# Performance work log

Hardware: AMD Instinct MI355X
Metric: run time of the kernel (lower is better)

## Reference

```python
import math
import jax, jax.numpy as jnp
import numpy as np

NUM_HEADS = 12
DIM = 1536
HEAD_DIM = DIM // NUM_HEADS  # 128
MAX_ATTN = 5632              # max_attention_size for window_size=(-1,-1)
EPS = 1e-6


def rmsnorm(x, g, eps=EPS):
    v = jnp.mean(jnp.square(x.astype(jnp.float32)), axis=-1, keepdims=True)
    return (x.astype(jnp.float32) * jax.lax.rsqrt(v + eps)).astype(x.dtype) * g


def causal_rope_apply(x, theta, start_frame, f, h, w):
    # x: [B, S, N, D] with S = f*h*w; theta: [1024, D//2] angles.
    b, s, n, d = x.shape
    c = d // 2
    ct = c - 2 * (c // 3)  # temporal rotary dims (22)
    ch = c // 3            # spatial rotary dims (21)
    ang = jnp.concatenate([
        jnp.broadcast_to(theta[start_frame:start_frame + f, :ct][:, None, None, :], (f, h, w, ct)),
        jnp.broadcast_to(theta[:h, ct:ct + ch][None, :, None, :], (f, h, w, ch)),
        jnp.broadcast_to(theta[:w, ct + ch:ct + 2 * ch][None, None, :, :], (f, h, w, ch)),
    ], axis=-1).reshape(s, c)
    cos = jnp.cos(ang)[None, :, None, :]  # [1, S, 1, c]
    sin = jnp.sin(ang)[None, :, None, :]
    xp = x.reshape(b, s, n, c, 2)
    xr, xi = xp[..., 0], xp[..., 1]
    out_r = xr * cos - xi * sin
    out_i = xr * sin + xi * cos
    return jnp.stack([out_r, out_i], axis=-1).reshape(b, s, n, d)


def setup_inputs() -> dict:
    key = jax.random.key(0)
    ks = jax.random.split(key, 12)
    B, F, H, W = 1, 2, 30, 52
    S = F * H * W  # 3120
    CACHE_LEN = 15600
    wscale = 0.02
    inp = {
        "x": jax.random.normal(ks[0], (B, S, DIM), jnp.float32),
        "freqs_theta": jax.random.uniform(ks[1], (1024, HEAD_DIM // 2), jnp.float32, 0.0, 2.0 * np.pi),
        "cache_k": jax.random.normal(ks[2], (B, CACHE_LEN, NUM_HEADS, HEAD_DIM), jnp.float32),
        "cache_v": jax.random.normal(ks[3], (B, CACHE_LEN, NUM_HEADS, HEAD_DIM), jnp.float32),
        "wq": jax.random.normal(ks[4], (DIM, DIM), jnp.float32) * wscale,
        "bq": jnp.zeros((DIM,), jnp.float32),
        "wk": jax.random.normal(ks[5], (DIM, DIM), jnp.float32) * wscale,
        "bk": jnp.zeros((DIM,), jnp.float32),
        "wv": jax.random.normal(ks[6], (DIM, DIM), jnp.float32) * wscale,
        "bv": jnp.zeros((DIM,), jnp.float32),
        "wo": jax.random.normal(ks[7], (DIM, DIM), jnp.float32) * wscale,
        "bo": jnp.zeros((DIM,), jnp.float32),
        "gq": jnp.ones((DIM,), jnp.float32),
        "gk": jnp.ones((DIM,), jnp.float32),
        "grid_f": F, "grid_h": H, "grid_w": W,
        "current_start": 7800,       # 5 frames already generated
        "global_end_index": 7800,
        "local_end_index": 7800,
    }
    return inp


def reference(x, freqs_theta, cache_k, cache_v, wq, bq, wk, bk, wv, bv, wo, bo,
              gq, gk, grid_f, grid_h, grid_w, current_start, global_end_index,
              local_end_index):
    B, S, D = x.shape
    N, Hd = NUM_HEADS, HEAD_DIM
    # qkv projections with RMS q/k norm (applied on full dim before head split)
    q = rmsnorm(x @ wq.T + bq, gq).reshape(B, S, N, Hd)
    k = rmsnorm(x @ wk.T + bk, gk).reshape(B, S, N, Hd)
    v = (x @ wv.T + bv).reshape(B, S, N, Hd)

    frame_seqlen = grid_h * grid_w
    start_frame = current_start // frame_seqlen
    rq = causal_rope_apply(q, freqs_theta, start_frame, grid_f, grid_h, grid_w)
    rk = causal_rope_apply(k, freqs_theta, start_frame, grid_f, grid_h, grid_w)

    # KV-cache scatter (static indices)
    current_end = current_start + S
    local_end = local_end_index + current_end - global_end_index
    local_start = local_end - S
    cache_k = cache_k.at[:, local_start:local_end].set(rk)
    cache_v = cache_v.at[:, local_start:local_end].set(v)

    # windowed attention over last MAX_ATTN cached tokens
    win_start = max(0, local_end - MAX_ATTN)
    kwin = cache_k[:, win_start:local_end]
    vwin = cache_v[:, win_start:local_end]
    scale = 1.0 / math.sqrt(Hd)
    scores = jnp.einsum('bqnd,bknd->bnqk', rq, kwin) * scale
    p = jax.nn.softmax(scores, axis=-1)
    o = jnp.einsum('bnqk,bknd->bqnd', p, vwin).reshape(B, S, D)
    return o @ wo.T + bo
```

## Files before the change

kernel.cpp:

```cpp
#include <hip/hip_runtime.h>

#define DIM 1536
#define NHEADS 12
#define HD 128
#define MAX_ATTN_WIN 5632
#define RMS_EPS 1e-6f
#define KWROWS 5632
#define NT_MAX 88
#define TILE_ELEMS 8192
#define KSTEPS 48
#define AREG 4096
#define BREG 8192

typedef unsigned short ushortT;
typedef __bf16 bf16x8 __attribute__((ext_vector_type(8)));
typedef float f32x4 __attribute__((ext_vector_type(4)));
typedef ushortT ushx8 __attribute__((ext_vector_type(8)));

__device__ __forceinline__ ushortT bf16r(float x) {
    union { float f; unsigned u; } v; v.f = x;
    unsigned r = v.u + 0x7FFFu + ((v.u >> 16) & 1u);
    return (ushortT)(r >> 16);
}
__device__ __forceinline__ ushx8 pack8(float4 a, float4 b) {
    ushx8 u;
    u[0] = bf16r(a.x); u[1] = bf16r(a.y); u[2] = bf16r(a.z); u[3] = bf16r(a.w);
    u[4] = bf16r(b.x); u[5] = bf16r(b.y); u[6] = bf16r(b.z); u[7] = bf16r(b.w);
    return u;
}

__device__ __forceinline__ void gload_lds16(const void* g, void* l) {
    typedef const __attribute__((address_space(1))) unsigned int GU;
    typedef __attribute__((address_space(3))) unsigned int LU;
    __builtin_amdgcn_global_load_lds((GU*)(unsigned long long)g,
                                     (LU*)(unsigned long long)l, 16, 0, 0);
}

__device__ __forceinline__ void pack_a_body(const float* __restrict__ X,
                                            ushortT* __restrict__ Ap,
                                            int M, int idx)
{
    int row = idx / 192, ch = idx - row * 192;
    int ks = ch >> 2, c = ch & 3;
    int mb = row >> 6, r = row & 63;
    ushx8 uh, ul;
    if (row < M) {
        const float* p = X + (size_t)row * DIM + (ch << 3);
        float4 a = *(const float4*)p;
        float4 b2 = *(const float4*)(p + 4);
        float xs[8] = {a.x, a.y, a.z, a.w, b2.x, b2.y, b2.z, b2.w};
        #pragma unroll
        for (int j = 0; j < 8; ++j) {
            ushortT hh = bf16r(xs[j]);
            union { unsigned u; float f; } w; w.u = ((unsigned)hh) << 16;
            uh[j] = hh; ul[j] = bf16r(xs[j] - w.f);
        }
    } else {
        #pragma unroll
        for (int j = 0; j < 8; ++j) { uh[j] = 0; ul[j] = 0; }
    }
    size_t base = (size_t)(mb * KSTEPS + ks) * AREG
                + r * 32 + ((c ^ ((r >> 1) & 3)) << 3);
    *(ushx8*)&Ap[base] = uh;
    *(ushx8*)&Ap[base + 2048] = ul;
}

__device__ __forceinline__ void pack_b_body(const float* __restrict__ W,
                                            ushortT* __restrict__ Bp, int idx)
{
    int row = idx / 192, ch = idx - row * 192;
    int ks = ch >> 2, c = ch & 3;
    int nb = row >> 7, rn = row & 127;
    const float* p = W + (size_t)row * DIM + (ch << 3);
    float4 a = *(const float4*)p;
    float4 b2 = *(const float4*)(p + 4);
    float xs[8] = {a.x, a.y, a.z, a.w, b2.x, b2.y, b2.z, b2.w};
    ushx8 uh, ul;
    #pragma unroll
    for (int j = 0; j < 8; ++j) {
        ushortT hh = bf16r(xs[j]);
        union { unsigned u; float f; } w; w.u = ((unsigned)hh) << 16;
        uh[j] = hh; ul[j] = bf16r(xs[j] - w.f);
    }
    size_t base = (size_t)(nb * KSTEPS + ks) * BREG
                + rn * 32 + ((c ^ ((rn >> 1) & 3)) << 3);
    *(ushx8*)&Bp[base] = uh;
    *(ushx8*)&Bp[base + 4096] = ul;
}

__global__ __launch_bounds__(256)
void pack1_kernel(const float* __restrict__ x, const float* __restrict__ wq,
                  const float* __restrict__ wk,
                  ushortT* __restrict__ Ap, ushortT* __restrict__ Bp0,
                  ushortT* __restrict__ Bp1, int M, int gA, int gB)
{
    int b = blockIdx.x;
    if (b < gA) {
        pack_a_body(x, Ap, M, b * 256 + threadIdx.x);
    } else if (b < gA + gB) {
        pack_b_body(wq, Bp0, (b - gA) * 256 + threadIdx.x);
    } else {
        pack_b_body(wk, Bp1, (b - gA - gB) * 256 + threadIdx.x);
    }
}

__global__ __launch_bounds__(256)
void pack2_kernel(const float* __restrict__ wv, const float* __restrict__ wo,
                  ushortT* __restrict__ Bp0, ushortT* __restrict__ Bp1, int gB)
{
    int b = blockIdx.x;
    if (b < gB) pack_b_body(wv, Bp0, b * 256 + threadIdx.x);
    else        pack_b_body(wo, Bp1, (b - gB) * 256 + threadIdx.x);
}

__global__ __launch_bounds__(256)
void pack_a_kernel(const float* __restrict__ X, ushortT* __restrict__ Ap,
                   int M, int Mpad)
{
    int idx = blockIdx.x * 256 + threadIdx.x;
    if (idx >= Mpad * 192) return;
    pack_a_body(X, Ap, M, idx);
}

template<int MODE>
__device__ __forceinline__
void gemm_body(const ushortT* __restrict__ Ap, const ushortT* __restrict__ Bp,
               const float* __restrict__ bias, float* __restrict__ C,
               ushortT* __restrict__ vwout, int M, int nmb, int orig,
               const int* __restrict__ p_cs, const int* __restrict__ p_ge,
               const int* __restrict__ p_le,
               ushortT (*As)[AREG], ushortT (*Bs)[BREG])
{
    const int tid = threadIdx.x;
    const int wid = tid >> 6, lane = tid & 63;
    const int lo = lane & 15, hi = lane >> 4;
    const int wm = wid >> 1, wn = wid & 1;

    const int nwg = nmb * (DIM / 128);
    const int xcd = orig & 7, linb = orig >> 3;
    const int qd = nwg >> 3, rr2 = nwg & 7;
    const int wg = (xcd < rr2 ? xcd * (qd + 1) : rr2 * (qd + 1) + (xcd - rr2) * qd) + linb;
    const int nb = wg / nmb, mb = wg - nb * nmb;
    const int m0 = mb << 6, n0 = nb << 7;

    f32x4 acc[2][4];
    #pragma unroll
    for (int i = 0; i < 2; ++i)
        #pragma unroll
        for (int j = 0; j < 4; ++j) acc[i][j] = (f32x4)(0.f);

    const ushortT* Asrc = Ap + (size_t)mb * (KSTEPS * AREG);
    const ushortT* Bsrc = Bp + (size_t)nb * (KSTEPS * BREG);
    const int lofs = lane << 3;
    const int aBase0 = (wid << 10) + lofs;
    const int aBase1 = aBase0 + 512;
    const int bBase  = (wid << 11) + lofs;

    gload_lds16(Asrc + aBase0, &As[0][aBase0]);
    gload_lds16(Asrc + aBase1, &As[0][aBase1]);
    #pragma unroll
    for (int i = 0; i < 4; ++i)
        gload_lds16(Bsrc + bBase + (i << 9), &Bs[0][bBase + (i << 9)]);

    const int cOff = ((hi ^ ((lo >> 1) & 3)) << 3);

    for (int ks = 0; ks < KSTEPS; ++ks) {
        const int b = ks & 1;
        __syncthreads();
        if (ks + 1 < KSTEPS) {
            const ushortT* as1 = Asrc + ((size_t)(ks + 1) << 12);
            const ushortT* bs1 = Bsrc + ((size_t)(ks + 1) << 13);
            gload_lds16(as1 + aBase0, &As[b ^ 1][aBase0]);
            gload_lds16(as1 + aBase1, &As[b ^ 1][aBase1]);
            #pragma unroll
            for (int i = 0; i < 4; ++i)
                gload_lds16(bs1 + bBase + (i << 9), &Bs[b ^ 1][bBase + (i << 9)]);
        }

        bf16x8 aH[2], aL[2];
        #pragma unroll
        for (int mf = 0; mf < 2; ++mf) {
            int r = (wm << 5) + (mf << 4) + lo;
            aH[mf] = *(const bf16x8*)&As[b][r * 32 + cOff];
            aL[mf] = *(const bf16x8*)&As[b][r * 32 + cOff + 2048];
        }
        #pragma unroll
        for (int nf = 0; nf < 4; ++nf) {
            int rn = (wn << 6) + (nf << 4) + lo;
            bf16x8 bH = *(const bf16x8*)&Bs[b][rn * 32 + cOff];
            bf16x8 bL = *(const bf16x8*)&Bs[b][rn * 32 + cOff + 4096];
            #pragma unroll
            for (int mf = 0; mf < 2; ++mf) {
                acc[mf][nf] = __builtin_amdgcn_mfma_f32_16x16x32_bf16(aH[mf], bH, acc[mf][nf], 0, 0, 0);
                acc[mf][nf] = __builtin_amdgcn_mfma_f32_16x16x32_bf16(aL[mf], bH, acc[mf][nf], 0, 0, 0);
                acc[mf][nf] = __builtin_amdgcn_mfma_f32_16x16x32_bf16(aH[mf], bL, acc[mf][nf], 0, 0, 0);
            }
        }
    }

    if (MODE == 0) {
        #pragma unroll
        for (int mf = 0; mf < 2; ++mf) {
            #pragma unroll
            for (int reg = 0; reg < 4; ++reg) {
                int gm = m0 + (wm << 5) + (mf << 4) + (hi << 2) + reg;
                if (gm < M) {
                    #pragma unroll
                    for (int nf = 0; nf < 4; ++nf) {
                        int gn = n0 + (wn << 6) + (nf << 4) + lo;
                        C[(size_t)gm * DIM + gn] = acc[mf][nf][reg] + bias[gn];
                    }
                }
            }
        }
    } else {
        const int S = M;
        const int local_end = p_le[0] + (p_cs[0] + S) - p_ge[0];
        int win_start = local_end - MAX_ATTN_WIN; if (win_start < 0) win_start = 0;
        const int vbase = (local_end - S) - win_start;
        #pragma unroll
        for (int mf = 0; mf < 2; ++mf) {
            #pragma unroll
            for (int reg = 0; reg < 4; ++reg) {
                int gm = m0 + (wm << 5) + (mf << 4) + (hi << 2) + reg;
                if (gm < M) {
                    #pragma unroll
                    for (int nf = 0; nf < 4; ++nf) {
                        int gn = n0 + (wn << 6) + (nf << 4) + lo;
                        int h2 = gn >> 7, d = gn & 127;
                        int pos = vbase + gm;
                        int tt = pos >> 6, w = pos & 63;
                        int swz = (((w >> 3) ^ (d & 7)) << 3) | (w & 7);
                        vwout[((size_t)h2 * NT_MAX + tt) * TILE_ELEMS + ((size_t)d << 6) + swz] =
                            bf16r(acc[mf][nf][reg] + bias[gn]);
                    }
                }
            }
        }
    }
}

__global__ __launch_bounds__(256, 3)
void gemm_qk_kernel(const ushortT* __restrict__ Ap,
                    const ushortT* __restrict__ BpQ, const ushortT* __restrict__ BpK,
                    const float* __restrict__ bq, const float* __restrict__ bk,
                    float* __restrict__ Cq, float* __restrict__ Ck,
                    int M, int nmb, int nwg)
{
    __shared__ __align__(16) ushortT As[2][AREG];
    __shared__ __align__(16) ushortT Bs[2][BREG];
    int gid = (int)blockIdx.x;
    if (gid < nwg)
        gemm_body<0>(Ap, BpQ, bq, Cq, nullptr, M, nmb, gid, nullptr, nullptr, nullptr, As, Bs);
    else
        gemm_body<0>(Ap, BpK, bk, Ck, nullptr, M, nmb, gid - nwg, nullptr, nullptr, nullptr, As, Bs);
}

template<int MODE>
__global__ __launch_bounds__(256, 3)
void gemm_single_kernel(const ushortT* __restrict__ Ap, const ushortT* __restrict__ Bp,
                        const float* __restrict__ bias, float* __restrict__ C,
                        ushortT* __restrict__ vwout, int M, int nmb,
                        const int* __restrict__ p_cs, const int* __restrict__ p_ge,
                        const int* __restrict__ p_le)
{
    __shared__ __align__(16) ushortT As[2][AREG];
    __shared__ __align__(16) ushortT Bs[2][BREG];
    gemm_body<MODE>(Ap, Bp, bias, C, vwout, M, nmb, (int)blockIdx.x,
                    p_cs, p_ge, p_le, As, Bs);
}

__global__ __launch_bounds__(256)
void rmsnorm_rope_kernel(float* __restrict__ qbuf, float* __restrict__ kbuf,
                         const float* __restrict__ gq, const float* __restrict__ gk,
                         const float* __restrict__ theta,
                         const int* __restrict__ p_gh, const int* __restrict__ p_gw,
                         const int* __restrict__ p_cs, int S)
{
    const int s = blockIdx.x;
    float* row = ((blockIdx.y == 0) ? qbuf : kbuf) + (size_t)s * DIM;
    const float* g = (blockIdx.y == 0) ? gq : gk;
    const int tid = threadIdx.x;

    float v[6];
    #pragma unroll
    for (int i = 0; i < 6; ++i) v[i] = row[tid * 6 + i];
    float ss = 0.f;
    #pragma unroll
    for (int i = 0; i < 6; ++i) ss += v[i] * v[i];
    #pragma unroll
    for (int off = 32; off > 0; off >>= 1) ss += __shfl_xor(ss, off, 64);

    __shared__ float red[4];
    if ((tid & 63) == 0) red[tid >> 6] = ss;
    __syncthreads();
    float tot = red[0] + red[1] + red[2] + red[3];
    float rs = rsqrtf(tot * (1.0f / DIM) + RMS_EPS);

    const int H = p_gh[0], W = p_gw[0];
    const int fs = p_cs[0] / (H * W);
    const int fr = s / (H * W);
    const int rem = s - fr * (H * W);
    const int hh = rem / W;
    const int ww = rem - hh * W;

    #pragma unroll
    for (int pi = 0; pi < 3; ++pi) {
        int p = tid * 3 + pi;
        int j = p & 63;
        float xr = v[pi * 2]     * rs * g[tid * 6 + pi * 2];
        float xi = v[pi * 2 + 1] * rs * g[tid * 6 + pi * 2 + 1];
        int rowi = (j < 22) ? (fs + fr) : ((j < 43) ? hh : ww);
        float ang = theta[rowi * 64 + j];
        float sn, cs;
        sincosf(ang, &sn, &cs);
        row[tid * 6 + pi * 2]     = xr * cs - xi * sn;
        row[tid * 6 + pi * 2 + 1] = xr * sn + xi * cs;
    }
}

__global__ __launch_bounds__(256)
void pack_kv_kernel(const float* __restrict__ cache_k, const float* __restrict__ k_lin,
                    const float* __restrict__ cache_v,
                    ushortT* __restrict__ kw, ushortT* __restrict__ vw,
                    const int* __restrict__ p_cs, const int* __restrict__ p_ge,
                    const int* __restrict__ p_le, int S)
{
    const int kt = blockIdx.x;
    const int local_end = p_le[0] + (p_cs[0] + S) - p_ge[0];
    int win_start = local_end - MAX_ATTN_WIN; if (win_start < 0) win_start = 0;
    const int L = local_end - win_start;
    const int cpart = (local_end - S) - win_start;

    if (blockIdx.y < NHEADS) {
        const int h = blockIdx.y;
        #pragma unroll
        for (int i = 0; i < 4; ++i) {
            int cid = (i << 8) + threadIdx.x;
            int r = cid >> 4, c = cid & 15;
            int pos = (kt << 6) + r;
            ushx8 u;
            if (pos < L) {
                const float* src = (pos < cpart)
                    ? &cache_k[(size_t)(win_start + pos) * DIM + h * HD + (c << 3)]
                    : &k_lin[(size_t)(pos - cpart) * DIM + h * HD + (c << 3)];
                float4 a = *(const float4*)src;
                float4 b = *(const float4*)(src + 4);
                u = pack8(a, b);
            } else {
                #pragma unroll
                for (int j = 0; j < 8; ++j) u[j] = 0;
            }
            *(ushx8*)&kw[(size_t)h * (KWROWS * HD) + (size_t)pos * HD + ((c ^ (r & 15)) << 3)] = u;
        }
    } else {
        const int h = blockIdx.y - NHEADS;
        const int tbase = kt << 6;
        if (tbase >= cpart && tbase + 64 <= L) return;

        __shared__ float tile[64 * 132];
        #pragma unroll
        for (int i = 0; i < 8; ++i) {
            int cid = (i << 8) + threadIdx.x;
            int r = cid >> 5, fc = cid & 31;
            int pos = tbase + r;
            float4 vv = (pos < cpart)
                ? *(const float4*)&cache_v[(size_t)(win_start + pos) * DIM + h * HD + (fc << 2)]
                : make_float4(0.f, 0.f, 0.f, 0.f);
            *(float4*)&tile[r * 132 + (fc << 2)] = vv;
        }
        __syncthreads();
        #pragma unroll
        for (int i = 0; i < 4; ++i) {
            int cid = (i << 8) + threadIdx.x;
            int d = cid >> 3, kc = cid & 7;
            int kglob = tbase + (kc << 3);
            ushx8 u;
            #pragma unroll
            for (int j = 0; j < 8; ++j)
                u[j] = bf16r(tile[((kc << 3) + j) * 132 + d]);
            size_t base = ((size_t)h * NT_MAX + kt) * TILE_ELEMS + ((size_t)d << 6)
                        + ((size_t)((kc ^ (d & 7)) << 3));
            if (kglob + 8 <= cpart) {
                *(ushx8*)&vw[base] = u;
            } else {
                #pragma unroll
                for (int j = 0; j < 8; ++j) {
                    int pos = kglob + j;
                    if (pos < cpart)      vw[base + j] = u[j];
                    else if (pos >= L)    vw[base + j] = 0;
                }
            }
        }
    }
}

__global__ __launch_bounds__(256, 3)
void attn_mfma5_kernel(const float* __restrict__ q_lin,
                       const ushortT* __restrict__ kw, const ushortT* __restrict__ vw,
                       float* __restrict__ obuf,
                       const int* __restrict__ p_cs, const int* __restrict__ p_ge,
                       const int* __restrict__ p_le, int S, int nqb)
{
    __shared__ __align__(16) ushortT Ks[TILE_ELEMS];
    __shared__ __align__(16) ushortT Vs[2][TILE_ELEMS];

    const int tid = threadIdx.x;
    const int wid = tid >> 6, lane = tid & 63;
    const int lo = lane & 15, hi = lane >> 4;

    const int nwg = nqb * NHEADS;
    const int orig = (int)blockIdx.x;
    const int xcd = orig & 7, linb = orig >> 3;
    const int qd = nwg >> 3, rr = nwg & 7;
    const int wg = (xcd < rr ? xcd * (qd + 1) : rr * (qd + 1) + (xcd - rr) * qd) + linb;
    const int h = wg / nqb;
    const int q0 = (wg - h * nqb) << 6;

    const int local_end = p_le[0] + (p_cs[0] + S) - p_ge[0];
    int win_start = local_end - MAX_ATTN_WIN; if (win_start < 0) win_start = 0;
    const int L = local_end - win_start;
    const int ntiles = (L + 63) >> 6;

    bf16x8 aQ[4];
    {
        int q = q0 + (wid << 4) + lo;
        if (q < S) {
            const float* qp = q_lin + (size_t)q * DIM + h * HD + (hi << 3);
            #pragma unroll
            for (int ks = 0; ks < 4; ++ks) {
                float4 a = *(const float4*)&qp[ks * 32];
                float4 b = *(const float4*)&qp[ks * 32 + 4];
                ushx8 u = pack8(a, b);
                aQ[ks] = *(bf16x8*)&u;
            }
        } else {
            ushx8 z;
            #pragma unroll
            for (int j = 0; j < 8; ++j) z[j] = 0;
            #pragma unroll
            for (int ks = 0; ks < 4; ++ks) aQ[ks] = *(bf16x8*)&z;
        }
    }

    f32x4 Oa[8];
    float lsum[4];
    #pragma unroll
    for (int i = 0; i < 8; ++i) Oa[i] = (f32x4)(0.f);
    #pragma unroll
    for (int i = 0; i < 4; ++i) lsum[i] = 0.f;

    const ushortT* kwp = kw + (size_t)h * (NT_MAX * TILE_ELEMS);
    const ushortT* vwp = vw + (size_t)h * (NT_MAX * TILE_ELEMS);
    const float scale = 0.08838834764831845f;
    const int pbase = wid << 11;
    const int sbase = (wid << 11) + (lane << 3);

    #pragma unroll
    for (int i = 0; i < 4; ++i) {
        gload_lds16(kwp + sbase + (i << 9), &Ks[sbase + (i << 9)]);
        gload_lds16(vwp + sbase + (i << 9), &Vs[0][sbase + (i << 9)]);
    }

    for (int t = 0; t < ntiles; ++t) {
        const int b = t & 1;
        __syncthreads();

        f32x4 Sa[4];
        #pragma unroll
        for (int nt = 0; nt < 4; ++nt) Sa[nt] = (f32x4)(0.f);
        #pragma unroll
        for (int nt = 0; nt < 4; ++nt) {
            const int kr = (nt << 4) + lo;
            #pragma unroll
            for (int ks = 0; ks < 4; ++ks) {
                bf16x8 bF = *(const bf16x8*)&Ks[kr * 128 + ((((ks << 2) + hi) ^ (kr & 15)) << 3)];
                Sa[nt] = __builtin_amdgcn_mfma_f32_16x16x32_bf16(aQ[ks], bF, Sa[nt], 0, 0, 0);
            }
        }

        __syncthreads();

        if (t + 1 < ntiles) {
            const ushortT* vsrc = vwp + ((size_t)(t + 1) << 13);
            ushortT* vdst = &Vs[b ^ 1][0];
            #pragma unroll
            for (int i = 0; i < 4; ++i)
                gload_lds16(vsrc + sbase + (i << 9), vdst + sbase + (i << 9));
        }

        const bool tail = (((t + 1) << 6) > L);
        #pragma unroll
        for (int nt = 0; nt < 4; ++nt) {
            #pragma unroll
            for (int reg = 0; reg < 4; ++reg) {
                float sv = Sa[nt][reg] * scale - 20.f;
                if (tail) {
                    int kg = (t << 6) + (nt << 4) + lo;
                    if (kg >= L) sv = -1e30f;
                }
                float p = __expf(sv);
                lsum[reg] += p;
                Sa[nt][reg] = p;
            }
        }

        #pragma unroll
        for (int nt = 0; nt < 4; ++nt) {
            #pragma unroll
            for (int reg = 0; reg < 4; ++reg) {
                int r = (hi << 2) + reg;
                int cc = (nt << 1) + (lo >> 3);
                Ks[pbase + (r << 6) + ((cc ^ (r & 7)) << 3) + (lo & 7)] = bf16r(Sa[nt][reg]);
            }
        }
        bf16x8 pF[2];
        #pragma unroll
        for (int ks = 0; ks < 2; ++ks)
            pF[ks] = *(const bf16x8*)&Ks[pbase + (lo << 6) + ((((ks << 2) + hi) ^ (lo & 7)) << 3)];

        asm volatile("s_waitcnt lgkmcnt(0)" ::: "memory");
        __builtin_amdgcn_sched_barrier(0);

        if (t + 1 < ntiles) {
            const ushortT* ksrc = kwp + ((size_t)(t + 1) << 13);
            #pragma unroll
            for (int i = 0; i < 4; ++i)
                gload_lds16(ksrc + sbase + (i << 9), &Ks[sbase + (i << 9)]);
        }

        #pragma unroll
        for (int nto = 0; nto < 8; ++nto) {
            const int d = (nto << 4) + lo;
            #pragma unroll
            for (int ks = 0; ks < 2; ++ks) {
                bf16x8 vF = *(const bf16x8*)&Vs[b][(d << 6) + ((((ks << 2) + hi) ^ (d & 7)) << 3)];
                Oa[nto] = __builtin_amdgcn_mfma_f32_16x16x32_bf16(pF[ks], vF, Oa[nto], 0, 0, 0);
            }
        }
    }

    #pragma unroll
    for (int reg = 0; reg < 4; ++reg) {
        #pragma unroll
        for (int off = 1; off < 16; off <<= 1)
            lsum[reg] += __shfl_xor(lsum[reg], off, 64);
    }
    #pragma unroll
    for (int reg = 0; reg < 4; ++reg) {
        int q = q0 + (wid << 4) + (hi << 2) + reg;
        if (q < S) {
            float inv = 1.f / lsum[reg];
            #pragma unroll
            for (int nto = 0; nto < 8; ++nto)
                obuf[(size_t)q * DIM + h * HD + (nto << 4) + lo] = Oa[nto][reg] * inv;
        }
    }
}

extern "C" void kernel_launch(void* const* d_in, const int* in_sizes, int n_in,
                              void* d_out, int out_size, void* d_ws, size_t ws_size,
                              hipStream_t stream)
{
    const float* x       = (const float*)d_in[0];
    const float* theta   = (const float*)d_in[1];
    const float* cache_k = (const float*)d_in[2];
    const float* cache_v = (const float*)d_in[3];
    const float* wq = (const float*)d_in[4];
    const float* bq = (const float*)d_in[5];
    const float* wk = (const float*)d_in[6];
    const float* bk = (const float*)d_in[7];
    const float* wv = (const float*)d_in[8];
    const float* bv = (const float*)d_in[9];
    const float* wo = (const float*)d_in[10];
    const float* bo = (const float*)d_in[11];
    const float* gq = (const float*)d_in[12];
    const float* gk = (const float*)d_in[13];
    const int* p_gh = (const int*)d_in[15];
    const int* p_gw = (const int*)d_in[16];
    const int* p_cs = (const int*)d_in[17];
    const int* p_ge = (const int*)d_in[18];
    const int* p_le = (const int*)d_in[19];

    const int S = in_sizes[0] / DIM;
    const int nmb = (S + 63) / 64;
    const int Mpad = nmb * 64;

    float* q_lin = (float*)d_ws;
    float* k_lin = q_lin + (size_t)S * DIM;
    float* o_buf = k_lin;
    ushortT* Ap  = (ushortT*)(k_lin + (size_t)S * DIM);
    ushortT* kw  = Ap;
    ushortT* vw  = Ap + (size_t)nmb * KSTEPS * AREG;
    ushortT* Bp0 = vw + (size_t)NHEADS * NT_MAX * TILE_ELEMS;
    ushortT* Bp1 = Bp0 + (size_t)NHEADS * KSTEPS * BREG;

    dim3 blk(256);
    const int nwgG = nmb * (DIM / 128);
    const int gA = (Mpad * 192) / 256;
    const int gB = (DIM * 192) / 256;

    pack1_kernel<<<gA + 2 * gB, blk, 0, stream>>>(x, wq, wk, Ap, Bp0, Bp1, S, gA, gB);
    gemm_qk_kernel<<<2 * nwgG, blk, 0, stream>>>(Ap, Bp0, Bp1, bq, bk,
                                                 q_lin, k_lin, S, nmb, nwgG);
    pack2_kernel<<<2 * gB, blk, 0, stream>>>(wv, wo, Bp0, Bp1, gB);
    gemm_single_kernel<1><<<nwgG, blk, 0, stream>>>(Ap, Bp0, bv, nullptr, vw,
                                                    S, nmb, p_cs, p_ge, p_le);

    rmsnorm_rope_kernel<<<dim3(S, 2), blk, 0, stream>>>(q_lin, k_lin, gq, gk, theta,
                                                        p_gh, p_gw, p_cs, S);

    pack_kv_kernel<<<dim3(NT_MAX, 2 * NHEADS), blk, 0, stream>>>(
        cache_k, k_lin, cache_v, kw, vw, p_cs, p_ge, p_le, S);

    const int nqb = (S + 63) / 64;
    attn_mfma5_kernel<<<dim3(nqb * NHEADS), blk, 0, stream>>>(
        q_lin, kw, vw, o_buf, p_cs, p_ge, p_le, S, nqb);

    pack_a_kernel<<<gA, blk, 0, stream>>>(o_buf, Ap, S, Mpad);
    gemm_single_kernel<0><<<nwgG, blk, 0, stream>>>(Ap, Bp1, bo, (float*)d_out, nullptr,
                                                    S, nmb, p_cs, p_ge, p_le);
}
```

Baseline: 681.2 us.

## Double query rows per attention workgroup to reuse K/V tiles

Each attention workgroup now handles 128 query rows instead of 64. Each wave owns two 16-row sub-blocks, so every K and V fragment read from LDS feeds two MFMAs. This halves global and LDS traffic for K/V per query and halves the number of workgroups. The cost is more registers per wave: occupancy drops to 2 blocks per SIMD, and there are fewer blocks (300) to spread across the CUs, so tail and balance effects are possible.

Result: slower. 712.6 us (+4.6%).

```diff
diff --git a/kernel.cpp b/kernel.cpp
--- a/kernel.cpp
+++ b/kernel.cpp
@@ -395,8 +395,8 @@
     }
 }
 
-__global__ __launch_bounds__(256, 3)
-void attn_mfma5_kernel(const float* __restrict__ q_lin,
+__global__ __launch_bounds__(256, 2)
+void attn_mfma6_kernel(const float* __restrict__ q_lin,
                        const ushortT* __restrict__ kw, const ushortT* __restrict__ vw,
                        float* __restrict__ obuf,
                        const int* __restrict__ p_cs, const int* __restrict__ p_ge,
@@ -415,16 +415,17 @@
     const int qd = nwg >> 3, rr = nwg & 7;
     const int wg = (xcd < rr ? xcd * (qd + 1) : rr * (qd + 1) + (xcd - rr) * qd) + linb;
     const int h = wg / nqb;
-    const int q0 = (wg - h * nqb) << 6;
+    const int q0 = (wg - h * nqb) << 7;
 
     const int local_end = p_le[0] + (p_cs[0] + S) - p_ge[0];
     int win_start = local_end - MAX_ATTN_WIN; if (win_start < 0) win_start = 0;
     const int L = local_end - win_start;
     const int ntiles = (L + 63) >> 6;
 
-    bf16x8 aQ[4];
-    {
-        int q = q0 + (wid << 4) + lo;
+    bf16x8 aQ[2][4];
+    #pragma unroll
+    for (int sub = 0; sub < 2; ++sub) {
+        int q = q0 + (wid << 5) + (sub << 4) + lo;
         if (q < S) {
             const float* qp = q_lin + (size_t)q * DIM + h * HD + (hi << 3);
             #pragma unroll
@@ -432,23 +433,26 @@
                 float4 a = *(const float4*)&qp[ks * 32];
                 float4 b = *(const float4*)&qp[ks * 32 + 4];
                 ushx8 u = pack8(a, b);
-                aQ[ks] = *(bf16x8*)&u;
+                aQ[sub][ks] = *(bf16x8*)&u;
             }
         } else {
             ushx8 z;
             #pragma unroll
             for (int j = 0; j < 8; ++j) z[j] = 0;
             #pragma unroll
-            for (int ks = 0; ks < 4; ++ks) aQ[ks] = *(bf16x8*)&z;
-        }
-    }
-
-    f32x4 Oa[8];
-    float lsum[4];
-    #pragma unroll
-    for (int i = 0; i < 8; ++i) Oa[i] = (f32x4)(0.f);
-    #pragma unroll
-    for (int i = 0; i < 4; ++i) lsum[i] = 0.f;
+            for (int ks = 0; ks < 4; ++ks) aQ[sub][ks] = *(bf16x8*)&z;
+        }
+    }
+
+    f32x4 Oa[2][8];
+    float lsum[2][4];
+    #pragma unroll
+    for (int sub = 0; sub < 2; ++sub) {
+        #pragma unroll
+        for (int i = 0; i < 8; ++i) Oa[sub][i] = (f32x4)(0.f);
+        #pragma unroll
+        for (int i = 0; i < 4; ++i) lsum[sub][i] = 0.f;
+    }
 
     const ushortT* kwp = kw + (size_t)h * (NT_MAX * TILE_ELEMS);
     const ushortT* vwp = vw + (size_t)h * (NT_MAX * TILE_ELEMS);
@@ -466,16 +470,17 @@
         const int b = t & 1;
         __syncthreads();
 
-        f32x4 Sa[4];
-        #pragma unroll
-        for (int nt = 0; nt < 4; ++nt) Sa[nt] = (f32x4)(0.f);
+        f32x4 Sa[2][4];
+        #pragma unroll
+        for (int nt = 0; nt < 4; ++nt) { Sa[0][nt] = (f32x4)(0.f); Sa[1][nt] = (f32x4)(0.f); }
         #pragma unroll
         for (int nt = 0; nt < 4; ++nt) {
             const int kr = (nt << 4) + lo;
             #pragma unroll
             for (int ks = 0; ks < 4; ++ks) {
                 bf16x8 bF = *(const bf16x8*)&Ks[kr * 128 + ((((ks << 2) + hi) ^ (kr & 15)) << 3)];
-                Sa[nt] = __builtin_amdgcn_mfma_f32_16x16x32_bf16(aQ[ks], bF, Sa[nt], 0, 0, 0);
+                Sa[0][nt] = __builtin_amdgcn_mfma_f32_16x16x32_bf16(aQ[0][ks], bF, Sa[0][nt], 0, 0, 0);
+                Sa[1][nt] = __builtin_amdgcn_mfma_f32_16x16x32_bf16(aQ[1][ks], bF, Sa[1][nt], 0, 0, 0);
             }
         }
 
@@ -491,33 +496,43 @@
 
         const bool tail = (((t + 1) << 6) > L);
         #pragma unroll
-        for (int nt = 0; nt < 4; ++nt) {
-            #pragma unroll
-            for (int reg = 0; reg < 4; ++reg) {
-                float sv = Sa[nt][reg] * scale - 20.f;
-                if (tail) {
-                    int kg = (t << 6) + (nt << 4) + lo;
-                    if (kg >= L) sv = -1e30f;
+        for (int sub = 0; sub < 2; ++sub) {
+            #pragma unroll
+            for (int nt = 0; nt < 4; ++nt) {
+                #pragma unroll
+                for (int reg = 0; reg < 4; ++reg) {
+                    float sv = Sa[sub][nt][reg] * scale - 20.f;
+                    if (tail) {
+                        int kg = (t << 6) + (nt << 4) + lo;
+                        if (kg >= L) sv = -1e30f;
+                    }
+                    float p = __expf(sv);
+                    lsum[sub][reg] += p;
+                    Sa[sub][nt][reg] = p;
                 }
-                float p = __expf(sv);
-                lsum[reg] += p;
-                Sa[nt][reg] = p;
-            }
-        }
-
-        #pragma unroll
-        for (int nt = 0; nt < 4; ++nt) {
-            #pragma unroll
-            for (int reg = 0; reg < 4; ++reg) {
-                int r = (hi << 2) + reg;
-                int cc = (nt << 1) + (lo >> 3);
-                Ks[pbase + (r << 6) + ((cc ^ (r & 7)) << 3) + (lo & 7)] = bf16r(Sa[nt][reg]);
-            }
-        }
-        bf16x8 pF[2];
-        #pragma unroll
-        for (int ks = 0; ks < 2; ++ks)
-            pF[ks] = *(const bf16x8*)&Ks[pbase + (lo << 6) + ((((ks << 2) + hi) ^ (lo & 7)) << 3)];
+            }
+        }
+
+        #pragma unroll
+        for (int sub = 0; sub < 2; ++sub) {
+            #pragma unroll
+            for (int nt = 0; nt < 4; ++nt) {
+                #pragma unroll
+                for (int reg = 0; reg < 4; ++reg) {
+                    int r = (hi << 2) + reg;
+                    int cc = (nt << 1) + (lo >> 3);
+                    Ks[pbase + (sub << 10) + (r << 6) + ((cc ^ (r & 7)) << 3) + (lo & 7)] =
+                        bf16r(Sa[sub][nt][reg]);
+                }
+            }
+        }
+        bf16x8 pF[2][2];
+        #pragma unroll
+        for (int sub = 0; sub < 2; ++sub)
+            #pragma unroll
+            for (int ks = 0; ks < 2; ++ks)
+                pF[sub][ks] = *(const bf16x8*)&Ks[pbase + (sub << 10) + (lo << 6)
+                                                 + ((((ks << 2) + hi) ^ (lo & 7)) << 3)];
 
         asm volatile("s_waitcnt lgkmcnt(0)" ::: "memory");
         __builtin_amdgcn_sched_barrier(0);
@@ -535,25 +550,29 @@
             #pragma unroll
             for (int ks = 0; ks < 2; ++ks) {
                 bf16x8 vF = *(const bf16x8*)&Vs[b][(d << 6) + ((((ks << 2) + hi) ^ (d & 7)) << 3)];
-                Oa[nto] = __builtin_amdgcn_mfma_f32_16x16x32_bf16(pF[ks], vF, Oa[nto], 0, 0, 0);
-            }
-        }
-    }
-
-    #pragma unroll
-    for (int reg = 0; reg < 4; ++reg) {
-        #pragma unroll
-        for (int off = 1; off < 16; off <<= 1)
-            lsum[reg] += __shfl_xor(lsum[reg], off, 64);
-    }
-    #pragma unroll
-    for (int reg = 0; reg < 4; ++reg) {
-        int q = q0 + (wid << 4) + (hi << 2) + reg;
-        if (q < S) {
-            float inv = 1.f / lsum[reg];
-            #pragma unroll
-            for (int nto = 0; nto < 8; ++nto)
-                obuf[(size_t)q * DIM + h * HD + (nto << 4) + lo] = Oa[nto][reg] * inv;
+                Oa[0][nto] = __builtin_amdgcn_mfma_f32_16x16x32_bf16(pF[0][ks], vF, Oa[0][nto], 0, 0, 0);
+                Oa[1][nto] = __builtin_amdgcn_mfma_f32_16x16x32_bf16(pF[1][ks], vF, Oa[1][nto], 0, 0, 0);
+            }
+        }
+    }
+
+    #pragma unroll
+    for (int sub = 0; sub < 2; ++sub) {
+        #pragma unroll
+        for (int reg = 0; reg < 4; ++reg) {
+            #pragma unroll
+            for (int off = 1; off < 16; off <<= 1)
+                lsum[sub][reg] += __shfl_xor(lsum[sub][reg], off, 64);
+        }
+        #pragma unroll
+        for (int reg = 0; reg < 4; ++reg) {
+            int q = q0 + (wid << 5) + (sub << 4) + (hi << 2) + reg;
+            if (q < S) {
+                float inv = 1.f / lsum[sub][reg];
+                #pragma unroll
+                for (int nto = 0; nto < 8; ++nto)
+                    obuf[(size_t)q * DIM + h * HD + (nto << 4) + lo] = Oa[sub][nto][reg] * inv;
+            }
         }
     }
 }
@@ -613,8 +632,8 @@
     pack_kv_kernel<<<dim3(NT_MAX, 2 * NHEADS), blk, 0, stream>>>(
         cache_k, k_lin, cache_v, kw, vw, p_cs, p_ge, p_le, S);
 
-    const int nqb = (S + 63) / 64;
-    attn_mfma5_kernel<<<dim3(nqb * NHEADS), blk, 0, stream>>>(
+    const int nqb = (S + 127) / 128;
+    attn_mfma6_kernel<<<dim3(nqb * NHEADS), blk, 0, stream>>>(
         q_lin, kw, vw, o_buf, p_cs, p_ge, p_le, S, nqb);
 
     pack_a_kernel<<<gA, blk, 0, stream>>>(o_buf, Ap, S, Mpad);
```

## Fuse QKV GEMMs, write K window from rmsnorm-rope, overlap wo packing with attention

Applied to the files above, without the earlier changes.

Packs wq/wk/wv in one launch and runs the Q, K and V projections as a single GEMM launch with three block ranges. The rmsnorm+RoPE kernel now converts the rotated K rows to bf16 and writes them straight into the swizzled attention K window, so the KV pack kernel only handles cached tokens and skips tiles made up entirely of new tokens. The wo weight packing is appended as extra blocks of the attention kernel to fill idle CUs. This removes launches and a full fp32 K round-trip, at the cost of extra shared memory in rmsnorm and a heavier, more mixed attention grid.

After: 656.7 us. 1.04x faster.

```diff
diff --git a/kernel.cpp b/kernel.cpp
--- a/kernel.cpp
+++ b/kernel.cpp
@@ -89,28 +89,18 @@
 }
 
 __global__ __launch_bounds__(256)
-void pack1_kernel(const float* __restrict__ x, const float* __restrict__ wq,
-                  const float* __restrict__ wk,
-                  ushortT* __restrict__ Ap, ushortT* __restrict__ Bp0,
-                  ushortT* __restrict__ Bp1, int M, int gA, int gB)
+void pack_all_kernel(const float* __restrict__ x, const float* __restrict__ wq,
+                     const float* __restrict__ wk, const float* __restrict__ wv,
+                     ushortT* __restrict__ Ap, ushortT* __restrict__ Bp0,
+                     ushortT* __restrict__ Bp1, ushortT* __restrict__ Bp2,
+                     int M, int gA, int gB)
 {
     int b = blockIdx.x;
-    if (b < gA) {
-        pack_a_body(x, Ap, M, b * 256 + threadIdx.x);
-    } else if (b < gA + gB) {
-        pack_b_body(wq, Bp0, (b - gA) * 256 + threadIdx.x);
-    } else {
-        pack_b_body(wk, Bp1, (b - gA - gB) * 256 + threadIdx.x);
-    }
-}
-
-__global__ __launch_bounds__(256)
-void pack2_kernel(const float* __restrict__ wv, const float* __restrict__ wo,
-                  ushortT* __restrict__ Bp0, ushortT* __restrict__ Bp1, int gB)
-{
-    int b = blockIdx.x;
-    if (b < gB) pack_b_body(wv, Bp0, b * 256 + threadIdx.x);
-    else        pack_b_body(wo, Bp1, (b - gB) * 256 + threadIdx.x);
+    if (b < gA) { pack_a_body(x, Ap, M, b * 256 + threadIdx.x); return; }
+    b -= gA;
+    if (b < gB)            pack_b_body(wq, Bp0, b * 256 + threadIdx.x);
+    else if (b < 2 * gB)   pack_b_body(wk, Bp1, (b - gB) * 256 + threadIdx.x);
+    else                   pack_b_body(wv, Bp2, (b - 2 * gB) * 256 + threadIdx.x);
 }
 
 __global__ __launch_bounds__(256)
@@ -241,19 +231,26 @@
 }
 
 __global__ __launch_bounds__(256, 3)
-void gemm_qk_kernel(const ushortT* __restrict__ Ap,
-                    const ushortT* __restrict__ BpQ, const ushortT* __restrict__ BpK,
-                    const float* __restrict__ bq, const float* __restrict__ bk,
-                    float* __restrict__ Cq, float* __restrict__ Ck,
-                    int M, int nmb, int nwg)
+void gemm_qkv_kernel(const ushortT* __restrict__ Ap,
+                     const ushortT* __restrict__ BpQ, const ushortT* __restrict__ BpK,
+                     const ushortT* __restrict__ BpV,
+                     const float* __restrict__ bq, const float* __restrict__ bk,
+                     const float* __restrict__ bv,
+                     float* __restrict__ Cq, float* __restrict__ Ck,
+                     ushortT* __restrict__ vw,
+                     int M, int nmb, int nwg,
+                     const int* __restrict__ p_cs, const int* __restrict__ p_ge,
+                     const int* __restrict__ p_le)
 {
     __shared__ __align__(16) ushortT As[2][AREG];
     __shared__ __align__(16) ushortT Bs[2][BREG];
     int gid = (int)blockIdx.x;
     if (gid < nwg)
         gemm_body<0>(Ap, BpQ, bq, Cq, nullptr, M, nmb, gid, nullptr, nullptr, nullptr, As, Bs);
+    else if (gid < 2 * nwg)
+        gemm_body<0>(Ap, BpK, bk, Ck, nullptr, M, nmb, gid - nwg, nullptr, nullptr, nullptr, As, Bs);
     else
-        gemm_body<0>(Ap, BpK, bk, Ck, nullptr, M, nmb, gid - nwg, nullptr, nullptr, nullptr, As, Bs);
+        gemm_body<1>(Ap, BpV, bv, nullptr, vw, M, nmb, gid - 2 * nwg, p_cs, p_ge, p_le, As, Bs);
 }
 
 template<int MODE>
@@ -272,14 +269,17 @@
 
 __global__ __launch_bounds__(256)
 void rmsnorm_rope_kernel(float* __restrict__ qbuf, float* __restrict__ kbuf,
+                         ushortT* __restrict__ kw,
                          const float* __restrict__ gq, const float* __restrict__ gk,
                          const float* __restrict__ theta,
                          const int* __restrict__ p_gh, const int* __restrict__ p_gw,
-                         const int* __restrict__ p_cs, int S)
+                         const int* __restrict__ p_cs, const int* __restrict__ p_ge,
+                         const int* __restrict__ p_le, int S)
 {
     const int s = blockIdx.x;
-    float* row = ((blockIdx.y == 0) ? qbuf : kbuf) + (size_t)s * DIM;
-    const float* g = (blockIdx.y == 0) ? gq : gk;
+    const bool isQ = (blockIdx.y == 0);
+    float* row = (isQ ? qbuf : kbuf) + (size_t)s * DIM;
+    const float* g = isQ ? gq : gk;
     const int tid = threadIdx.x;
 
     float v[6];
@@ -292,6 +292,7 @@
     for (int off = 32; off > 0; off >>= 1) ss += __shfl_xor(ss, off, 64);
 
     __shared__ float red[4];
+    __shared__ ushortT krow[DIM];
     if ((tid & 63) == 0) red[tid >> 6] = ss;
     __syncthreads();
     float tot = red[0] + red[1] + red[2] + red[3];
@@ -304,6 +305,7 @@
     const int hh = rem / W;
     const int ww = rem - hh * W;
 
+    float out[6];
     #pragma unroll
     for (int pi = 0; pi < 3; ++pi) {
         int p = tid * 3 + pi;
@@ -314,17 +316,35 @@
         float ang = theta[rowi * 64 + j];
         float sn, cs;
         sincosf(ang, &sn, &cs);
-        row[tid * 6 + pi * 2]     = xr * cs - xi * sn;
-        row[tid * 6 + pi * 2 + 1] = xr * sn + xi * cs;
+        out[pi * 2]     = xr * cs - xi * sn;
+        out[pi * 2 + 1] = xr * sn + xi * cs;
+    }
+
+    if (isQ) {
+        #pragma unroll
+        for (int i = 0; i < 6; ++i) row[tid * 6 + i] = out[i];
+    } else {
+        #pragma unroll
+        for (int i = 0; i < 6; ++i) krow[tid * 6 + i] = bf16r(out[i]);
+        __syncthreads();
+        const int local_end = p_le[0] + (p_cs[0] + S) - p_ge[0];
+        int win_start = local_end - MAX_ATTN_WIN; if (win_start < 0) win_start = 0;
+        const int cpart = (local_end - S) - win_start;
+        const int pos = cpart + s;
+        if (pos >= 0 && tid < 192) {
+            int h2 = tid >> 4, c = tid & 15;
+            ushx8 u = *(const ushx8*)&krow[h2 * 128 + (c << 3)];
+            *(ushx8*)&kw[(size_t)h2 * (KWROWS * HD) + (size_t)pos * HD
+                         + ((c ^ (pos & 15)) << 3)] = u;
+        }
     }
 }
 
 __global__ __launch_bounds__(256)
-void pack_kv_kernel(const float* __restrict__ cache_k, const float* __restrict__ k_lin,
-                    const float* __restrict__ cache_v,
-                    ushortT* __restrict__ kw, ushortT* __restrict__ vw,
-                    const int* __restrict__ p_cs, const int* __restrict__ p_ge,
-                    const int* __restrict__ p_le, int S)
+void pack_kvcache_kernel(const float* __restrict__ cache_k, const float* __restrict__ cache_v,
+                         ushortT* __restrict__ kw, ushortT* __restrict__ vw,
+                         const int* __restrict__ p_cs, const int* __restrict__ p_ge,
+                         const int* __restrict__ p_le, int S)
 {
     const int kt = blockIdx.x;
     const int local_end = p_le[0] + (p_cs[0] + S) - p_ge[0];
@@ -334,16 +354,17 @@
 
     if (blockIdx.y < NHEADS) {
         const int h = blockIdx.y;
+        const int tbase = kt << 6;
+        if (tbase >= cpart && tbase + 64 <= L) return;
         #pragma unroll
         for (int i = 0; i < 4; ++i) {
             int cid = (i << 8) + threadIdx.x;
             int r = cid >> 4, c = cid & 15;
-            int pos = (kt << 6) + r;
+            int pos = tbase + r;
+            if (pos >= cpart && pos < L) continue;
             ushx8 u;
-            if (pos < L) {
-                const float* src = (pos < cpart)
-                    ? &cache_k[(size_t)(win_start + pos) * DIM + h * HD + (c << 3)]
-                    : &k_lin[(size_t)(pos - cpart) * DIM + h * HD + (c << 3)];
+            if (pos < cpart) {
+                const float* src = &cache_k[(size_t)(win_start + pos) * DIM + h * HD + (c << 3)];
                 float4 a = *(const float4*)src;
                 float4 b = *(const float4*)(src + 4);
                 u = pack8(a, b);
@@ -351,7 +372,7 @@
                 #pragma unroll
                 for (int j = 0; j < 8; ++j) u[j] = 0;
             }
-            *(ushx8*)&kw[(size_t)h * (KWROWS * HD) + (size_t)pos * HD + ((c ^ (r & 15)) << 3)] = u;
+            *(ushx8*)&kw[(size_t)h * (KWROWS * HD) + (size_t)pos * HD + ((c ^ (pos & 15)) << 3)] = u;
         }
     } else {
         const int h = blockIdx.y - NHEADS;
@@ -396,14 +417,20 @@
 }
 
 __global__ __launch_bounds__(256, 3)
-void attn_mfma5_kernel(const float* __restrict__ q_lin,
-                       const ushortT* __restrict__ kw, const ushortT* __restrict__ vw,
-                       float* __restrict__ obuf,
-                       const int* __restrict__ p_cs, const int* __restrict__ p_ge,
-                       const int* __restrict__ p_le, int S, int nqb)
+void attn_wo_kernel(const float* __restrict__ q_lin,
+                    const ushortT* __restrict__ kw, const ushortT* __restrict__ vw,
+                    float* __restrict__ obuf,
+                    const float* __restrict__ wo, ushortT* __restrict__ BpO,
+                    const int* __restrict__ p_cs, const int* __restrict__ p_ge,
+                    const int* __restrict__ p_le, int S, int nqb, int nattn)
 {
     __shared__ __align__(16) ushortT Ks[TILE_ELEMS];
     __shared__ __align__(16) ushortT Vs[2][TILE_ELEMS];
+
+    if ((int)blockIdx.x >= nattn) {
+        pack_b_body(wo, BpO, ((int)blockIdx.x - nattn) * 256 + threadIdx.x);
+        return;
+    }
 
     const int tid = threadIdx.x;
     const int wid = tid >> 6, lane = tid & 63;
@@ -594,30 +621,30 @@
     ushortT* vw  = Ap + (size_t)nmb * KSTEPS * AREG;
     ushortT* Bp0 = vw + (size_t)NHEADS * NT_MAX * TILE_ELEMS;
     ushortT* Bp1 = Bp0 + (size_t)NHEADS * KSTEPS * BREG;
+    ushortT* Bp2 = Bp1 + (size_t)NHEADS * KSTEPS * BREG;
 
     dim3 blk(256);
     const int nwgG = nmb * (DIM / 128);
     const int gA = (Mpad * 192) / 256;
     const int gB = (DIM * 192) / 256;
 
-    pack1_kernel<<<gA + 2 * gB, blk, 0, stream>>>(x, wq, wk, Ap, Bp0, Bp1, S, gA, gB);
-    gemm_qk_kernel<<<2 * nwgG, blk, 0, stream>>>(Ap, Bp0, Bp1, bq, bk,
-                                                 q_lin, k_lin, S, nmb, nwgG);
-    pack2_kernel<<<2 * gB, blk, 0, stream>>>(wv, wo, Bp0, Bp1, gB);
-    gemm_single_kernel<1><<<nwgG, blk, 0, stream>>>(Ap, Bp0, bv, nullptr, vw,
+    pack_all_kernel<<<gA + 3 * gB, blk, 0, stream>>>(x, wq, wk, wv,
+                                                     Ap, Bp0, Bp1, Bp2, S, gA, gB);
+    gemm_qkv_kernel<<<3 * nwgG, blk, 0, stream>>>(Ap, Bp0, Bp1, Bp2, bq, bk, bv,
+                                                  q_lin, k_lin, vw, S, nmb, nwgG,
+                                                  p_cs, p_ge, p_le);
+
+    rmsnorm_rope_kernel<<<dim3(S, 2), blk, 0, stream>>>(q_lin, k_lin, kw, gq, gk, theta,
+                                                        p_gh, p_gw, p_cs, p_ge, p_le, S);
+
+    pack_kvcache_kernel<<<dim3(NT_MAX, 2 * NHEADS), blk, 0, stream>>>(
+        cache_k, cache_v, kw, vw, p_cs, p_ge, p_le, S);
+
+    const int nqb = (S + 63) / 64;
+    attn_wo_kernel<<<dim3(nqb * NHEADS + gB), blk, 0, stream>>>(
+        q_lin, kw, vw, o_buf, wo, Bp0, p_cs, p_ge, p_le, S, nqb, nqb * NHEADS);
+
+    pack_a_kernel<<<gA, blk, 0, stream>>>(o_buf, Ap, S, Mpad);
+    gemm_single_kernel<0><<<nwgG, blk, 0, stream>>>(Ap, Bp0, bo, (float*)d_out, nullptr,
                                                     S, nmb, p_cs, p_ge, p_le);
-
-    rmsnorm_rope_kernel<<<dim3(S, 2), blk, 0, stream>>>(q_lin, k_lin, gq, gk, theta,
-                                                        p_gh, p_gw, p_cs, S);
-
-    pack_kv_kernel<<<dim3(NT_MAX, 2 * NHEADS), blk, 0, stream>>>(
-        cache_k, k_lin, cache_v, kw, vw, p_cs, p_ge, p_le, S);
-
-    const int nqb = (S + 63) / 64;
-    attn_mfma5_kernel<<<dim3(nqb * NHEADS), blk, 0, stream>>>(
-        q_lin, kw, vw, o_buf, p_cs, p_ge, p_le, S, nqb);
-
-    pack_a_kernel<<<gA, blk, 0, stream>>>(o_buf, Ap, S, Mpad);
-    gemm_single_kernel<0><<<nwgG, blk, 0, stream>>>(Ap, Bp1, bo, (float*)d_out, nullptr,
-                                                    S, nmb, p_cs, p_ge, p_le);
-}
+}
```
